# Performance work log

Hardware: AMD Instinct MI355X
Metric: run time of the kernel (lower is better)

## Reference

```python
import jax, jax.numpy as jnp
import numpy as np

N, E, G = 50000, 640000, 2000
F_NODE, F_EDGE, H, L, T = 64, 16, 128, 2, 2


def _seg_softmax(logits, idx, num_seg):
    # logits: [E], idx: [E] -> softmax per segment
    m = jax.ops.segment_max(logits, idx, num_segments=num_seg)
    e = jnp.exp(logits - m[idx])
    s = jax.ops.segment_sum(e, idx, num_segments=num_seg)
    return e / (s[idx] + 1e-16)


def _gru(x, h, Wih, Whh, bih, bhh):
    gi = x @ Wih + bih
    gh = h @ Whh + bhh
    ir, iz, inn = jnp.split(gi, 3, axis=-1)
    hr, hz, hn = jnp.split(gh, 3, axis=-1)
    r = jax.nn.sigmoid(ir + hr)
    z = jax.nn.sigmoid(iz + hz)
    n = jnp.tanh(inn + r * hn)
    return (1.0 - z) * n + z * h


def setup_inputs() -> dict:
    key = jax.random.key(0)
    ks = jax.random.split(key, 30)
    s = 0.05
    inp = {
        'x': jax.random.normal(ks[0], (N, F_NODE), jnp.float32),
        'edge_index': jax.random.randint(ks[1], (2, E), 0, N, jnp.int32),
        'edge_attr': jax.random.normal(ks[2], (E, F_EDGE), jnp.float32),
        'batch': jnp.sort(jax.random.randint(ks[3], (N,), 0, G, jnp.int32)),
        'emb_W': jax.random.normal(ks[4], (F_NODE, H), jnp.float32) * s,
        'emb_b': jnp.zeros((H,), jnp.float32),
        'attW1': jax.random.normal(ks[5], (L, 2 * H + F_EDGE, H), jnp.float32) * s,
        'attb1': jnp.zeros((L, H), jnp.float32),
        'attW2': jax.random.normal(ks[6], (L, H, 1), jnp.float32) * s,
        'attb2': jnp.zeros((L, 1), jnp.float32),
        'mlpW': jax.random.normal(ks[7], (L, H + F_EDGE, H), jnp.float32) * s,
        'mlpb': jnp.zeros((L, H), jnp.float32),
        'gru_Wih': jax.random.normal(ks[8], (L, H, 3 * H), jnp.float32) * s,
        'gru_Whh': jax.random.normal(ks[9], (L, H, 3 * H), jnp.float32) * s,
        'gru_bih': jnp.zeros((L, 3 * H), jnp.float32),
        'gru_bhh': jnp.zeros((L, 3 * H), jnp.float32),
        'gattW1': jax.random.normal(ks[10], (H, H), jnp.float32) * s,
        'gattb1': jnp.zeros((H,), jnp.float32),
        'gattW2': jax.random.normal(ks[11], (H, 1), jnp.float32) * s,
        'gattb2': jnp.zeros((1,), jnp.float32),
        'ggru_Wih': jax.random.normal(ks[12], (H, 3 * H), jnp.float32) * s,
        'ggru_Whh': jax.random.normal(ks[13], (H, 3 * H), jnp.float32) * s,
        'ggru_bih': jnp.zeros((3 * H,), jnp.float32),
        'ggru_bhh': jnp.zeros((3 * H,), jnp.float32),
    }
    return inp


def reference(x, edge_index, edge_attr, batch, emb_W, emb_b, attW1, attb1,
              attW2, attb2, mlpW, mlpb, gru_Wih, gru_Whh, gru_bih, gru_bhh,
              gattW1, gattb1, gattW2, gattb2, ggru_Wih, ggru_Whh, ggru_bih,
              ggru_bhh):
    src, dst = edge_index[0], edge_index[1]  # PyG: x_j = x[src], x_i = x[dst]
    h = jax.nn.relu(x @ emb_W + emb_b)  # [N, H]
    for l in range(L):
        x_i, x_j = h[dst], h[src]                       # [E, H] gathers
        cat = jnp.concatenate([x_i, x_j, edge_attr], axis=-1)  # [E, 2H+F_e]
        a = jax.nn.leaky_relu(cat @ attW1[l] + attb1[l], 0.2) @ attW2[l] + attb2[l]
        alpha = _seg_softmax(a[:, 0], dst, N)[:, None]  # segment softmax over dst
        msg = jax.nn.relu(jnp.concatenate([x_j, edge_attr], axis=-1) @ mlpW[l] + mlpb[l])
        aggr = jax.ops.segment_sum(alpha * msg, dst, num_segments=N)  # [N, H]
        h = _gru(aggr, h, gru_Wih[l], gru_Whh[l], gru_bih[l], gru_bhh[l])
    g = jax.ops.segment_sum(h, batch, num_segments=G)  # global_add_pool [G, H]
    for _ in range(T):
        s = jnp.tanh(h @ gattW1 + gattb1) @ gattW2 + gattb2  # [N, 1]
        att = _seg_softmax(s[:, 0], batch, G)[:, None]
        ctx = jax.ops.segment_sum(att * h, batch, num_segments=G)
        g = _gru(ctx, g, ggru_Wih, ggru_Whh, ggru_bih, ggru_bhh)
    return g
```

## Files before the change

kernel.cpp:

```cpp
#include <hip/hip_runtime.h>
#include <hip/hip_bf16.h>
#include <math.h>

#define N_NODES 50000
#define N_EDGES 640000
#define N_GRAPHS 2000
#define FN 64
#define FE 16
#define H 128
#define NL 2
#define SCB 1024

typedef __attribute__((ext_vector_type(8))) short short8;
typedef __attribute__((ext_vector_type(4))) float float4v;
typedef __hip_bfloat16 bf16;

static constexpr size_t AL = 256;
static constexpr size_t alup(size_t x) { return (x + AL - 1) & ~(AL - 1); }

static constexpr size_t SZ_HF    = (size_t)N_NODES * H * 4;
static constexpr size_t SZ_HB    = (size_t)N_NODES * H * 2;
static constexpr size_t SZ_XB    = (size_t)N_NODES * FN * 2;
static constexpr size_t SZ_PQMB  = (size_t)N_NODES * 384 * 2;
static constexpr size_t SZ_GH    = (size_t)N_NODES * 384 * 4;
static constexpr size_t SZ_GI    = (size_t)N_NODES * 384 * 4;
static constexpr size_t SZ_AGB   = (size_t)N_NODES * H * 2;
static constexpr size_t SZ_NF    = (size_t)N_NODES * 4;
static constexpr size_t SZ_WT    = (size_t)768 * 128 * 2;
static constexpr size_t SZ_WIHT  = (size_t)384 * 128 * 2;
static constexpr size_t SZ_EMBT  = (size_t)128 * 64 * 2;
static constexpr size_t SZ_BBIG  = (size_t)768 * 4;
static constexpr size_t SZ_G128  = (size_t)N_GRAPHS * 128 * 4;
static constexpr size_t SZ_G384  = (size_t)N_GRAPHS * 384 * 4;
static constexpr size_t SZ_GF    = (size_t)N_GRAPHS * 4;
static constexpr size_t SZ_CSE   = (size_t)N_EDGES * 8;
static constexpr size_t SZ_BSUM  = 256 * 4;

static constexpr size_t OFF_H0    = 0;
static constexpr size_t OFF_H1    = alup(OFF_H0 + SZ_HF);
static constexpr size_t OFF_H0B   = alup(OFF_H1 + SZ_HF);
static constexpr size_t OFF_H1B   = alup(OFF_H0B + SZ_HB);
static constexpr size_t OFF_XB    = alup(OFF_H1B + SZ_HB);
static constexpr size_t OFF_PQMB  = alup(OFF_XB + SZ_XB);
static constexpr size_t OFF_GH    = alup(OFF_PQMB + SZ_PQMB);
static constexpr size_t OFF_GI    = alup(OFF_GH + SZ_GH);
static constexpr size_t OFF_AGB   = alup(OFF_GI + SZ_GI);
static constexpr size_t OFF_ES    = alup(OFF_AGB + SZ_AGB);
static constexpr size_t OFF_WT    = alup(OFF_ES + SZ_NF);
static constexpr size_t OFF_WIHT  = alup(OFF_WT + SZ_WT);
static constexpr size_t OFF_EMBT  = alup(OFF_WIHT + SZ_WIHT);
static constexpr size_t OFF_BBIG  = alup(OFF_EMBT + SZ_EMBT);
static constexpr size_t OFF_G0    = alup(OFF_BBIG + SZ_BBIG);
static constexpr size_t OFF_GA    = alup(OFF_G0 + SZ_G128);
static constexpr size_t OFF_CTX   = alup(OFF_GA + SZ_G128);
static constexpr size_t OFF_GICTX = alup(OFF_CTX + SZ_G128);
static constexpr size_t OFF_GHB   = alup(OFF_GICTX + SZ_G384);
static constexpr size_t OFF_GSUM  = alup(OFF_GHB + SZ_G384);
static constexpr size_t OFF_DEG   = alup(OFF_GSUM + SZ_GF);
static constexpr size_t OFF_OFFS  = alup(OFF_DEG + SZ_NF);
static constexpr size_t OFF_CUR   = alup(OFF_OFFS + SZ_NF + 4);
static constexpr size_t OFF_CSE   = alup(OFF_CUR + SZ_NF);
static constexpr size_t OFF_GHIST = alup(OFF_CSE + SZ_CSE);
static constexpr size_t OFF_GOFFS = alup(OFF_GHIST + SZ_GF);
static constexpr size_t OFF_BSUM  = alup(OFF_GOFFS + SZ_GF + 4);
static constexpr size_t TOTAL_WS  = alup(OFF_BSUM + SZ_BSUM);

__device__ unsigned char g_afp_ws[TOTAL_WS];

__device__ inline float bf2f(unsigned short u) {
    unsigned int x = ((unsigned int)u) << 16;
    return __uint_as_float(x);
}

template<int K>
__global__ __launch_bounds__(256) void gemm_mfma(
    const bf16* __restrict__ Abf, const bf16* __restrict__ Btbf,
    const float* __restrict__ bias, float* __restrict__ C,
    bf16* __restrict__ Cb, bf16* __restrict__ Cb2,
    int M, int Ncol, int mode)
{
    const unsigned short* A  = (const unsigned short*)Abf;
    const unsigned short* Bt = (const unsigned short*)Btbf;
    const int l  = threadIdx.x & 63;
    const int w  = threadIdx.x >> 6;
    const int wm = w >> 1, wn = w & 1;
    const int row0 = blockIdx.x * 64 + wm * 32;
    const int col0 = blockIdx.y * 64 + wn * 32;
    const int lr = l & 15;
    const int lk = (l >> 4) * 8;
    float4v acc[2][2] = {};
    #pragma unroll
    for (int k0 = 0; k0 < K; k0 += 32) {
        short8 a[2], b[2];
        #pragma unroll
        for (int i = 0; i < 2; ++i) {
            int r = row0 + i * 16 + lr;
            if (r >= M) r = M - 1;
            a[i] = *(const short8*)(A + (size_t)r * K + k0 + lk);
        }
        #pragma unroll
        for (int j = 0; j < 2; ++j) {
            int c = col0 + j * 16 + lr;
            b[j] = *(const short8*)(Bt + (size_t)c * K + k0 + lk);
        }
        #pragma unroll
        for (int i = 0; i < 2; ++i)
            #pragma unroll
            for (int j = 0; j < 2; ++j)
                acc[i][j] = __builtin_amdgcn_mfma_f32_16x16x32_bf16(a[i], b[j], acc[i][j], 0, 0, 0);
    }
    const int orow = (l >> 4) * 4;
    const int ocol = l & 15;
    #pragma unroll
    for (int i = 0; i < 2; ++i) {
        #pragma unroll
        for (int j = 0; j < 2; ++j) {
            const int gc = col0 + j * 16 + ocol;
            const float bi = bias ? bias[gc] : 0.f;
            #pragma unroll
            for (int r = 0; r < 4; ++r) {
                const int gr = row0 + i * 16 + orow + r;
                if (gr >= M) continue;
                float v = acc[i][j][r] + bi;
                if (mode & 1) v = fmaxf(v, 0.f);
                if (mode & 2) {
                    if (gc < 384) Cb[(size_t)gr * 384 + gc] = __float2bfloat16(v);
                    else          Cb2[(size_t)gr * 384 + (gc - 384)] = __float2bfloat16(v);
                } else if (mode & 8) {
                    Cb[(size_t)gr * Ncol + gc] = __float2bfloat16(v);
                } else {
                    C[(size_t)gr * Ncol + gc] = v;
                    if (mode & 4) Cb[(size_t)gr * Ncol + gc] = __float2bfloat16(v);
                }
            }
        }
    }
}

__global__ __launch_bounds__(256) void gemm_gru(
    const bf16* __restrict__ Abf, const bf16* __restrict__ Btbf,
    const float* __restrict__ bias, const bf16* __restrict__ ghb,
    const bf16* __restrict__ holdb, bf16* __restrict__ hnewb, int M)
{
    const unsigned short* A  = (const unsigned short*)Abf;
    const unsigned short* Bt = (const unsigned short*)Btbf;
    const unsigned short* gh = (const unsigned short*)ghb;
    const unsigned short* hold = (const unsigned short*)holdb;
    const int l  = threadIdx.x & 63;
    const int w  = threadIdx.x >> 6;
    const int row0 = blockIdx.x * 64 + w * 16;
    const int lr = l & 15;
    const int lk = (l >> 4) * 8;
    float4v acc[24] = {};
    #pragma unroll
    for (int k0 = 0; k0 < 128; k0 += 32) {
        int r = row0 + lr;
        if (r >= M) r = M - 1;
        short8 a = *(const short8*)(A + (size_t)r * 128 + k0 + lk);
        #pragma unroll
        for (int j = 0; j < 24; ++j) {
            short8 b = *(const short8*)(Bt + (size_t)(j * 16 + lr) * 128 + k0 + lk);
            acc[j] = __builtin_amdgcn_mfma_f32_16x16x32_bf16(a, b, acc[j], 0, 0, 0);
        }
    }
    const int orow = (l >> 4) * 4;
    const int ocol = l & 15;
    #pragma unroll
    for (int a_ = 0; a_ < 8; ++a_) {
        const int c = a_ * 16 + ocol;
        const float bir = bias[c], biz = bias[c + 128], bin = bias[c + 256];
        #pragma unroll
        for (int r = 0; r < 4; ++r) {
            const int gr = row0 + orow + r;
            if (gr >= M) continue;
            float ir = acc[a_][r] + bir;
            float iz = acc[a_ + 8][r] + biz;
            float in = acc[a_ + 16][r] + bin;
            const unsigned short* ghp = gh + (size_t)gr * 384;
            float hr = bf2f(ghp[c]);
            float hz = bf2f(ghp[128 + c]);
            float hn = bf2f(ghp[256 + c]);
            float rg = 1.f / (1.f + __expf(-(ir + hr)));
            float zg = 1.f / (1.f + __expf(-(iz + hz)));
            float ng = tanhf(in + rg * hn);
            float hv = bf2f(hold[(size_t)gr * 128 + c]);
            float o = (1.f - zg) * ng + zg * hv;
            hnewb[(size_t)gr * 128 + c] = __float2bfloat16(o);
        }
    }
}

#define GBM 64
#define GBN 64
#define GBK 32
__global__ __launch_bounds__(256) void gemm_f32(
    const float* __restrict__ A, const float* __restrict__ B,
    const float* __restrict__ bias, float* __restrict__ C,
    int M, int K, int Ncol)
{
    __shared__ float As[GBK][GBM + 4];
    __shared__ float Bs[GBK][GBN + 4];
    const int tx = threadIdx.x & 15;
    const int ty = threadIdx.x >> 4;
    const int row0 = blockIdx.x * GBM;
    const int col0 = blockIdx.y * GBN;
    float acc[4][4] = {};
    for (int k0 = 0; k0 < K; k0 += GBK) {
        for (int i = threadIdx.x; i < GBM * GBK; i += 256) {
            int r = i / GBK, c = i % GBK;
            float v = 0.f;
            if (row0 + r < M) v = A[(size_t)(row0 + r) * K + k0 + c];
            As[c][r] = v;
        }
        for (int i = threadIdx.x; i < GBK * GBN; i += 256) {
            int r = i / GBN, c = i % GBN;
            float v = 0.f;
            if (col0 + c < Ncol) v = B[(size_t)(k0 + r) * Ncol + col0 + c];
            Bs[r][c] = v;
        }
        __syncthreads();
        #pragma unroll
        for (int k = 0; k < GBK; ++k) {
            float a[4], b[4];
            #pragma unroll
            for (int i = 0; i < 4; ++i) a[i] = As[k][ty * 4 + i];
            #pragma unroll
            for (int j = 0; j < 4; ++j) b[j] = Bs[k][tx * 4 + j];
            #pragma unroll
            for (int i = 0; i < 4; ++i)
                #pragma unroll
                for (int j = 0; j < 4; ++j)
                    acc[i][j] = fmaf(a[i], b[j], acc[i][j]);
        }
        __syncthreads();
    }
    #pragma unroll
    for (int i = 0; i < 4; ++i) {
        int r = row0 + ty * 4 + i;
        if (r >= M) continue;
        #pragma unroll
        for (int j = 0; j < 4; ++j) {
            int c = col0 + tx * 4 + j;
            if (c >= Ncol) continue;
            C[(size_t)r * Ncol + c] = acc[i][j] + (bias ? bias[c] : 0.f);
        }
    }
}

__global__ void pack_weights_bt(const float* __restrict__ attW1,
                                const float* __restrict__ mlpW,
                                const float* __restrict__ whh,
                                const float* __restrict__ attb1,
                                const float* __restrict__ mlpb,
                                const float* __restrict__ bhh,
                                bf16* __restrict__ wt, float* __restrict__ bbig)
{
    int idx = blockIdx.x * blockDim.x + threadIdx.x;
    if (idx >= 768 * 128) return;
    int j = idx >> 7, k = idx & 127;
    float v;
    if (j < 128)      v = attW1[k * 128 + j];
    else if (j < 256) v = attW1[(128 + k) * 128 + (j - 128)];
    else if (j < 384) v = mlpW[k * 128 + (j - 256)];
    else              v = whh[k * 384 + (j - 384)];
    wt[idx] = __float2bfloat16(v);
    if (k == 0) {
        float b;
        if (j < 128)      b = attb1[j];
        else if (j < 256) b = 0.f;
        else if (j < 384) b = mlpb[j - 256];
        else              b = bhh[j - 384];
        bbig[j] = b;
    }
}

__global__ void transpose_cast(const float* __restrict__ in, bf16* __restrict__ out,
                               int K, int Ncol)
{
    int idx = blockIdx.x * blockDim.x + threadIdx.x;
    if (idx >= K * Ncol) return;
    int k = idx / Ncol, j = idx % Ncol;
    out[(size_t)j * K + k] = __float2bfloat16(in[idx]);
}

__global__ void cast_bf16_kernel(const float* __restrict__ in, bf16* __restrict__ out, int n)
{
    int idx = blockIdx.x * blockDim.x + threadIdx.x;
    if (idx < n) out[idx] = __float2bfloat16(in[idx]);
}

__global__ void hist_dst_kernel(const int* __restrict__ ei, int* __restrict__ deg) {
    int e = blockIdx.x * blockDim.x + threadIdx.x;
    if (e < N_EDGES) atomicAdd(&deg[ei[N_EDGES + e]], 1);
}
__global__ void hist_batch_kernel(const int* __restrict__ batch, int* __restrict__ hist) {
    int n = blockIdx.x * blockDim.x + threadIdx.x;
    if (n < N_NODES) atomicAdd(&hist[batch[n]], 1);
}

__global__ __launch_bounds__(1024) void scan_local(const int* __restrict__ in,
        int* __restrict__ out, int* __restrict__ bsum, int n)
{
    __shared__ int buf[SCB];
    int i = blockIdx.x * SCB + threadIdx.x;
    int v = (i < n) ? in[i] : 0;
    buf[threadIdx.x] = v;
    __syncthreads();
    #pragma unroll
    for (int off = 1; off < SCB; off <<= 1) {
        int t = (threadIdx.x >= off) ? buf[threadIdx.x - off] : 0;
        __syncthreads();
        buf[threadIdx.x] += t;
        __syncthreads();
    }
    if (i < n) out[i] = buf[threadIdx.x] - v;
    if (threadIdx.x == SCB - 1) bsum[blockIdx.x] = buf[SCB - 1];
}
__global__ __launch_bounds__(1024) void scan_bsum(int* __restrict__ bsum, int nb,
        int* __restrict__ total_dst)
{
    __shared__ int buf[SCB];
    int v = (threadIdx.x < nb) ? bsum[threadIdx.x] : 0;
    buf[threadIdx.x] = v;
    __syncthreads();
    #pragma unroll
    for (int off = 1; off < SCB; off <<= 1) {
        int t = (threadIdx.x >= off) ? buf[threadIdx.x - off] : 0;
        __syncthreads();
        buf[threadIdx.x] += t;
        __syncthreads();
    }
    if (threadIdx.x < nb) bsum[threadIdx.x] = buf[threadIdx.x] - v;
    if (threadIdx.x == 0) *total_dst = buf[SCB - 1];
}
__global__ __launch_bounds__(1024) void scan_addoff(int* __restrict__ out,
        const int* __restrict__ bsum, int n)
{
    int i = blockIdx.x * SCB + threadIdx.x;
    if (i < n) out[i] += bsum[blockIdx.x];
}

__global__ void scatter_cse_kernel(const int* __restrict__ ei, const int* __restrict__ offs,
                                   int* __restrict__ cur, int2* __restrict__ cse) {
    int e = blockIdx.x * blockDim.x + threadIdx.x;
    if (e >= N_EDGES) return;
    int d = ei[N_EDGES + e];
    int pos = offs[d] + atomicAdd(&cur[d], 1);
    cse[pos] = make_int2(ei[e], e);
}

__global__ __launch_bounds__(256, 2) void edge_fused_kernel(
    const bf16* __restrict__ pqm_b,
    const int2* __restrict__ cse, const float* __restrict__ ea,
    const float* __restrict__ w1c_g, const float* __restrict__ w2_g,
    const float* __restrict__ b2_g, const float* __restrict__ mlpw2_g,
    const int* __restrict__ offs, bf16* __restrict__ aggrb)
{
    const unsigned short* pqm = (const unsigned short*)pqm_b;
    const int wv = threadIdx.x >> 6, lane = threadIdx.x & 63;
    const int c0 = lane * 2;
    float w1r[16][2], wmr[16][2];
    #pragma unroll
    for (int k = 0; k < 16; ++k) {
        w1r[k][0] = w1c_g[k * 128 + c0];
        w1r[k][1] = w1c_g[k * 128 + c0 + 1];
        wmr[k][0] = mlpw2_g[k * 128 + c0];
        wmr[k][1] = mlpw2_g[k * 128 + c0 + 1];
    }
    const float w20 = w2_g[c0], w21 = w2_g[c0 + 1];
    const float b2 = b2_g[0];
    const int d = __builtin_amdgcn_readfirstlane(blockIdx.x * 4 + wv);
    if (d >= N_NODES) return;

    const ushort2 pu = *(const ushort2*)(pqm + (size_t)d * 384 + c0);
    const float p0 = bf2f(pu.x), p1 = bf2f(pu.y);
    float acc0 = 0.f, acc1 = 0.f, ssum = 0.f;
    const int b = offs[d], en = offs[d + 1];
    if (b < en) {
        int2 se = cse[b];
        const unsigned short* ps = pqm + (size_t)se.x * 384;
        ushort2 qu = *(const ushort2*)(ps + 128 + c0);
        ushort2 mu = *(const ushort2*)(ps + 256 + c0);
        const float4* eap = (const float4*)(ea + (size_t)se.y * 16);
        float4 e0 = eap[0], e1 = eap[1], e2 = eap[2], e3 = eap[3];
        for (int i = b; i < en; ++i) {
            float t0 = p0 + bf2f(qu.x), t1 = p1 + bf2f(qu.y);
            float m0 = bf2f(mu.x), m1 = bf2f(mu.y);
            float er[16];
            er[0]=e0.x; er[1]=e0.y; er[2]=e0.z; er[3]=e0.w;
            er[4]=e1.x; er[5]=e1.y; er[6]=e1.z; er[7]=e1.w;
            er[8]=e2.x; er[9]=e2.y; er[10]=e2.z; er[11]=e2.w;
            er[12]=e3.x; er[13]=e3.y; er[14]=e3.z; er[15]=e3.w;
            if (i + 1 < en) {
                se = cse[i + 1];
                const unsigned short* psn = pqm + (size_t)se.x * 384;
                qu = *(const ushort2*)(psn + 128 + c0);
                mu = *(const ushort2*)(psn + 256 + c0);
                const float4* eapn = (const float4*)(ea + (size_t)se.y * 16);
                e0 = eapn[0]; e1 = eapn[1]; e2 = eapn[2]; e3 = eapn[3];
            }
            #pragma unroll
            for (int k = 0; k < 16; ++k) {
                t0 = fmaf(er[k], w1r[k][0], t0);
                t1 = fmaf(er[k], w1r[k][1], t1);
                m0 = fmaf(er[k], wmr[k][0], m0);
                m1 = fmaf(er[k], wmr[k][1], m1);
            }
            float a0 = (t0 > 0.f) ? t0 : 0.2f * t0;
            float a1 = (t1 > 0.f) ? t1 : 0.2f * t1;
            float sp = a0 * w20 + a1 * w21;
            #pragma unroll
            for (int off = 32; off; off >>= 1) sp += __shfl_xor(sp, off);
            const float ex = __expf(sp + b2);
            ssum += ex;
            acc0 = fmaf(ex, fmaxf(m0, 0.f), acc0);
            acc1 = fmaf(ex, fmaxf(m1, 0.f), acc1);
        }
    }
    const float inv = 1.f / (ssum + 1e-16f);
    bf16* outp = aggrb + (size_t)d * 128 + c0;
    outp[0] = __float2bfloat16(acc0 * inv);
    outp[1] = __float2bfloat16(acc1 * inv);
}

__global__ void gru_elem_kernel(const float* __restrict__ gi,
                                const float* __restrict__ gh,
                                const float* __restrict__ hold, float* __restrict__ hnew,
                                int rows)
{
    int idx = blockIdx.x * blockDim.x + threadIdx.x;
    if (idx >= rows * H) return;
    int r = idx >> 7, c = idx & 127;
    float ir = gi[(size_t)r * 384 + c];
    float iz = gi[(size_t)r * 384 + 128 + c];
    float in = gi[(size_t)r * 384 + 256 + c];
    float hr = gh[(size_t)r * 384 + c];
    float hz = gh[(size_t)r * 384 + 128 + c];
    float hn = gh[(size_t)r * 384 + 256 + c];
    float rg = 1.f / (1.f + __expf(-(ir + hr)));
    float zg = 1.f / (1.f + __expf(-(iz + hz)));
    float ng = tanhf(in + rg * hn);
    float hv = hold[idx];
    hnew[idx] = (1.f - zg) * ng + zg * hv;
}

__global__ __launch_bounds__(128) void graph_pool_sum(
    const bf16* __restrict__ hb, const int* __restrict__ goffs, float* __restrict__ g0)
{
    const unsigned short* h = (const unsigned short*)hb;
    int g = blockIdx.x, c = threadIdx.x;
    int b = goffs[g], e2 = goffs[g + 1];
    float acc = 0.f;
    for (int i = b; i < e2; ++i) acc += bf2f(h[(size_t)i * 128 + c]);
    g0[(size_t)g * 128 + c] = acc;
}

__global__ __launch_bounds__(256) void node_score2_kernel(
    const float* __restrict__ hW1, const float* __restrict__ W2,
    const float* __restrict__ b2, const int* __restrict__ batch,
    float* __restrict__ es, float* __restrict__ gsum)
{
    const int wv = threadIdx.x >> 6, lane = threadIdx.x & 63;
    const int n = blockIdx.x * 4 + wv;
    if (n >= N_NODES) return;
    const int c0 = lane * 2;
    float sp = tanhf(hW1[(size_t)n * 128 + c0]) * W2[c0]
             + tanhf(hW1[(size_t)n * 128 + c0 + 1]) * W2[c0 + 1];
    #pragma unroll
    for (int off = 32; off; off >>= 1) sp += __shfl_xor(sp, off);
    if (lane == 0) {
        float ex = __expf(sp + b2[0]);
        es[n] = ex;
        atomicAdd(&gsum[batch[n]], ex);
    }
}

__global__ __launch_bounds__(128) void graph_ctx_kernel(
    const bf16* __restrict__ hb, const int* __restrict__ goffs,
    const float* __restrict__ es, const float* __restrict__ gsum,
    float* __restrict__ ctx)
{
    const unsigned short* h = (const unsigned short*)hb;
    int g = blockIdx.x, c = threadIdx.x;
    float invs = 1.f / (gsum[g] + 1e-16f);
    int b = goffs[g], e2 = goffs[g + 1];
    float acc = 0.f;
    for (int i = b; i < e2; ++i) acc = fmaf(es[i] * invs, bf2f(h[(size_t)i * 128 + c]), acc);
    ctx[(size_t)g * 128 + c] = acc;
}

extern "C" void kernel_launch(void* const* d_in, const int* in_sizes, int n_in,
                              void* d_out, int out_size, void* d_ws, size_t ws_size,
                              hipStream_t stream) {
    const float* x      = (const float*)d_in[0];
    const int*   ei     = (const int*)d_in[1];
    const float* ea     = (const float*)d_in[2];
    const int*   batch  = (const int*)d_in[3];
    const float* embW   = (const float*)d_in[4];
    const float* embB   = (const float*)d_in[5];
    const float* attW1  = (const float*)d_in[6];
    const float* attb1  = (const float*)d_in[7];
    const float* attW2  = (const float*)d_in[8];
    const float* attb2  = (const float*)d_in[9];
    const float* mlpW   = (const float*)d_in[10];
    const float* mlpb   = (const float*)d_in[11];
    const float* gWih   = (const float*)d_in[12];
    const float* gWhh   = (const float*)d_in[13];
    const float* gbih   = (const float*)d_in[14];
    const float* gbhh   = (const float*)d_in[15];
    const float* gattW1 = (const float*)d_in[16];
    const float* gattb1 = (const float*)d_in[17];
    const float* gattW2 = (const float*)d_in[18];
    const float* gattb2 = (const float*)d_in[19];
    const float* ggWih  = (const float*)d_in[20];
    const float* ggWhh  = (const float*)d_in[21];
    const float* ggbih  = (const float*)d_in[22];
    const float* ggbhh  = (const float*)d_in[23];
    float* out = (float*)d_out;

    void* basep = nullptr;
    (void)hipGetSymbolAddress(&basep, HIP_SYMBOL(g_afp_ws));
    char* base = (char*)basep;
    bf16*  h0b   = (bf16*)(base + OFF_H0B);
    bf16*  h1b   = (bf16*)(base + OFF_H1B);
    bf16*  xb    = (bf16*)(base + OFF_XB);
    bf16*  pqmb  = (bf16*)(base + OFF_PQMB);
    bf16*  ghx   = (bf16*)(base + OFF_GH);
    float* hW1   = (float*)(base + OFF_GI);
    bf16*  aggrb = (bf16*)(base + OFF_AGB);
    float* es    = (float*)(base + OFF_ES);
    bf16*  wt    = (bf16*)(base + OFF_WT);
    bf16*  wiht  = (bf16*)(base + OFF_WIHT);
    bf16*  embt  = (bf16*)(base + OFF_EMBT);
    float* bbig  = (float*)(base + OFF_BBIG);
    float* g0b   = (float*)(base + OFF_G0);
    float* gAb   = (float*)(base + OFF_GA);
    float* ctx   = (float*)(base + OFF_CTX);
    float* gictx = (float*)(base + OFF_GICTX);
    float* ghr   = (float*)(base + OFF_GHB);
    float* gsum  = (float*)(base + OFF_GSUM);
    int*   deg   = (int*)(base + OFF_DEG);
    int*   offs  = (int*)(base + OFF_OFFS);
    int*   cur   = (int*)(base + OFF_CUR);
    int2*  cse   = (int2*)(base + OFF_CSE);
    int*   ghist = (int*)(base + OFF_GHIST);
    int*   goffs = (int*)(base + OFF_GOFFS);
    int*   bsum  = (int*)(base + OFF_BSUM);

    (void)hipMemsetAsync(deg, 0, SZ_NF, stream);
    (void)hipMemsetAsync(cur, 0, SZ_NF, stream);
    (void)hipMemsetAsync(ghist, 0, SZ_GF, stream);
    (void)hipMemsetAsync(gsum, 0, SZ_GF, stream);

    const int nbN = (N_NODES + SCB - 1) / SCB;
    const int nbG = (N_GRAPHS + SCB - 1) / SCB;

    hist_dst_kernel<<<(N_EDGES + 255) / 256, 256, 0, stream>>>(ei, deg);
    scan_local<<<nbN, SCB, 0, stream>>>(deg, offs, bsum, N_NODES);
    scan_bsum<<<1, SCB, 0, stream>>>(bsum, nbN, offs + N_NODES);
    scan_addoff<<<nbN, SCB, 0, stream>>>(offs, bsum, N_NODES);
    scatter_cse_kernel<<<(N_EDGES + 255) / 256, 256, 0, stream>>>(ei, offs, cur, cse);
    hist_batch_kernel<<<(N_NODES + 255) / 256, 256, 0, stream>>>(batch, ghist);
    scan_local<<<nbG, SCB, 0, stream>>>(ghist, goffs, bsum, N_GRAPHS);
    scan_bsum<<<1, SCB, 0, stream>>>(bsum, nbG, goffs + N_GRAPHS);
    scan_addoff<<<nbG, SCB, 0, stream>>>(goffs, bsum, N_GRAPHS);

    cast_bf16_kernel<<<(N_NODES * FN + 255) / 256, 256, 0, stream>>>(x, xb, N_NODES * FN);
    transpose_cast<<<(FN * 128 + 255) / 256, 256, 0, stream>>>(embW, embt, FN, 128);

    {
        dim3 g((N_NODES + 63) / 64, 128 / 64);
        gemm_mfma<64><<<g, 256, 0, stream>>>(xb, embt, embB, nullptr, h0b, nullptr,
                                             N_NODES, 128, 1 | 8);
    }

    bf16* hcurb = h0b;
    bf16* hnextb = h1b;
    for (int l = 0; l < NL; ++l) {
        pack_weights_bt<<<(768 * 128 + 255) / 256, 256, 0, stream>>>(
            attW1 + (size_t)l * 272 * 128, mlpW + (size_t)l * 144 * 128,
            gWhh + (size_t)l * 128 * 384, attb1 + l * 128, mlpb + l * 128,
            gbhh + l * 384, wt, bbig);
        {
            dim3 g((N_NODES + 63) / 64, 768 / 64);
            gemm_mfma<128><<<g, 256, 0, stream>>>(hcurb, wt, bbig, nullptr, pqmb, ghx,
                                                  N_NODES, 768, 2);
        }
        edge_fused_kernel<<<(N_NODES + 3) / 4, 256, 0, stream>>>(
            pqmb, cse, ea, attW1 + (size_t)l * 272 * 128 + 256 * 128,
            attW2 + (size_t)l * 128, attb2 + l,
            mlpW + (size_t)l * 144 * 128 + 128 * 128,
            offs, aggrb);
        transpose_cast<<<(128 * 384 + 255) / 256, 256, 0, stream>>>(
            gWih + (size_t)l * 128 * 384, wiht, 128, 384);
        gemm_gru<<<(N_NODES + 63) / 64, 256, 0, stream>>>(
            aggrb, wiht, gbih + l * 384, ghx, hcurb, hnextb, N_NODES);
        bf16* tb = hcurb; hcurb = hnextb; hnextb = tb;
    }

    graph_pool_sum<<<N_GRAPHS, 128, 0, stream>>>(hcurb, goffs, g0b);
    transpose_cast<<<(128 * 128 + 255) / 256, 256, 0, stream>>>(gattW1, wiht, 128, 128);
    {
        dim3 g((N_NODES + 63) / 64, 128 / 64);
        gemm_mfma<128><<<g, 256, 0, stream>>>(hcurb, wiht, gattb1, hW1, nullptr, nullptr,
                                              N_NODES, 128, 0);
    }
    node_score2_kernel<<<(N_NODES + 3) / 4, 256, 0, stream>>>(
        hW1, gattW2, gattb2, batch, es, gsum);
    graph_ctx_kernel<<<N_GRAPHS, 128, 0, stream>>>(hcurb, goffs, es, gsum, ctx);

    dim3 gg((N_GRAPHS + 63) / 64, 384 / 64);
    gemm_f32<<<gg, 256, 0, stream>>>(ctx, ggWih, ggbih, gictx, N_GRAPHS, H, 384);
    gemm_f32<<<gg, 256, 0, stream>>>(g0b, ggWhh, ggbhh, ghr, N_GRAPHS, H, 384);
    gru_elem_kernel<<<((size_t)N_GRAPHS * H + 255) / 256, 256, 0, stream>>>(
        gictx, ghr, g0b, gAb, N_GRAPHS);
    gemm_f32<<<gg, 256, 0, stream>>>(gAb, ggWhh, ggbhh, ghr, N_GRAPHS, H, 384);
    gru_elem_kernel<<<((size_t)N_GRAPHS * H + 255) / 256, 256, 0, stream>>>(
        gictx, ghr, gAb, out, N_GRAPHS);
}
```

Before: 916.3 us.

## Reorder edge attrs into CSR order, interleave q/m columns, pack edge weights

The scatter step now writes edge attributes into a dst-sorted contiguous buffer, so the edge kernel reads them sequentially instead of gathering by edge id. The GEMM output interleaves the q and m columns so one 8-byte load fetches both per lane. The edge weights are pre-packed as float4 per lane, and the edge loop processes four edges per batch so four shuffle reductions run together. The attention score GEMM output becomes bf16 and the memsets are merged into one, trading an extra copy of the edge attributes and lower-precision hW1 for less scattered memory traffic.

```diff
diff --git a/kernel.cpp b/kernel.cpp
--- a/kernel.cpp
+++ b/kernel.cpp
@@ -18,51 +18,53 @@
 static constexpr size_t AL = 256;
 static constexpr size_t alup(size_t x) { return (x + AL - 1) & ~(AL - 1); }
 
-static constexpr size_t SZ_HF    = (size_t)N_NODES * H * 4;
 static constexpr size_t SZ_HB    = (size_t)N_NODES * H * 2;
 static constexpr size_t SZ_XB    = (size_t)N_NODES * FN * 2;
 static constexpr size_t SZ_PQMB  = (size_t)N_NODES * 384 * 2;
-static constexpr size_t SZ_GH    = (size_t)N_NODES * 384 * 4;
-static constexpr size_t SZ_GI    = (size_t)N_NODES * 384 * 4;
+static constexpr size_t SZ_GHX   = (size_t)N_NODES * 384 * 2;
+static constexpr size_t SZ_HW1B  = (size_t)N_NODES * H * 2;
 static constexpr size_t SZ_AGB   = (size_t)N_NODES * H * 2;
 static constexpr size_t SZ_NF    = (size_t)N_NODES * 4;
 static constexpr size_t SZ_WT    = (size_t)768 * 128 * 2;
 static constexpr size_t SZ_WIHT  = (size_t)384 * 128 * 2;
 static constexpr size_t SZ_EMBT  = (size_t)128 * 64 * 2;
+static constexpr size_t SZ_WPK   = (size_t)16 * 256 * 4;
 static constexpr size_t SZ_BBIG  = (size_t)768 * 4;
 static constexpr size_t SZ_G128  = (size_t)N_GRAPHS * 128 * 4;
 static constexpr size_t SZ_G384  = (size_t)N_GRAPHS * 384 * 4;
 static constexpr size_t SZ_GF    = (size_t)N_GRAPHS * 4;
-static constexpr size_t SZ_CSE   = (size_t)N_EDGES * 8;
+static constexpr size_t SZ_CSRC  = (size_t)N_EDGES * 4 + 64;
+static constexpr size_t SZ_EAC   = (size_t)N_EDGES * 64;
 static constexpr size_t SZ_BSUM  = 256 * 4;
 
-static constexpr size_t OFF_H0    = 0;
-static constexpr size_t OFF_H1    = alup(OFF_H0 + SZ_HF);
-static constexpr size_t OFF_H0B   = alup(OFF_H1 + SZ_HF);
+static constexpr size_t OFF_H0B   = 0;
 static constexpr size_t OFF_H1B   = alup(OFF_H0B + SZ_HB);
 static constexpr size_t OFF_XB    = alup(OFF_H1B + SZ_HB);
 static constexpr size_t OFF_PQMB  = alup(OFF_XB + SZ_XB);
-static constexpr size_t OFF_GH    = alup(OFF_PQMB + SZ_PQMB);
-static constexpr size_t OFF_GI    = alup(OFF_GH + SZ_GH);
-static constexpr size_t OFF_AGB   = alup(OFF_GI + SZ_GI);
+static constexpr size_t OFF_GHX   = alup(OFF_PQMB + SZ_PQMB);
+static constexpr size_t OFF_HW1B  = alup(OFF_GHX + SZ_GHX);
+static constexpr size_t OFF_AGB   = alup(OFF_HW1B + SZ_HW1B);
 static constexpr size_t OFF_ES    = alup(OFF_AGB + SZ_AGB);
 static constexpr size_t OFF_WT    = alup(OFF_ES + SZ_NF);
 static constexpr size_t OFF_WIHT  = alup(OFF_WT + SZ_WT);
 static constexpr size_t OFF_EMBT  = alup(OFF_WIHT + SZ_WIHT);
-static constexpr size_t OFF_BBIG  = alup(OFF_EMBT + SZ_EMBT);
+static constexpr size_t OFF_WPK   = alup(OFF_EMBT + SZ_EMBT);
+static constexpr size_t OFF_BBIG  = alup(OFF_WPK + SZ_WPK);
 static constexpr size_t OFF_G0    = alup(OFF_BBIG + SZ_BBIG);
 static constexpr size_t OFF_GA    = alup(OFF_G0 + SZ_G128);
 static constexpr size_t OFF_CTX   = alup(OFF_GA + SZ_G128);
 static constexpr size_t OFF_GICTX = alup(OFF_CTX + SZ_G128);
-static constexpr size_t OFF_GHB   = alup(OFF_GICTX + SZ_G384);
-static constexpr size_t OFF_GSUM  = alup(OFF_GHB + SZ_G384);
-static constexpr size_t OFF_DEG   = alup(OFF_GSUM + SZ_GF);
-static constexpr size_t OFF_OFFS  = alup(OFF_DEG + SZ_NF);
-static constexpr size_t OFF_CUR   = alup(OFF_OFFS + SZ_NF + 4);
-static constexpr size_t OFF_CSE   = alup(OFF_CUR + SZ_NF);
-static constexpr size_t OFF_GHIST = alup(OFF_CSE + SZ_CSE);
-static constexpr size_t OFF_GOFFS = alup(OFF_GHIST + SZ_GF);
-static constexpr size_t OFF_BSUM  = alup(OFF_GOFFS + SZ_GF + 4);
+static constexpr size_t OFF_GHR   = alup(OFF_GICTX + SZ_G384);
+static constexpr size_t OFF_DEG   = alup(OFF_GHR + SZ_G384);
+static constexpr size_t OFF_CUR   = alup(OFF_DEG + SZ_NF);
+static constexpr size_t OFF_GHIST = alup(OFF_CUR + SZ_NF);
+static constexpr size_t OFF_GSUM  = alup(OFF_GHIST + SZ_GF);
+static constexpr size_t SZ_ZERO   = OFF_GSUM + SZ_GF - OFF_DEG;
+static constexpr size_t OFF_OFFS  = alup(OFF_GSUM + SZ_GF);
+static constexpr size_t OFF_GOFFS = alup(OFF_OFFS + SZ_NF + 4);
+static constexpr size_t OFF_CSRC  = alup(OFF_GOFFS + SZ_GF + 4);
+static constexpr size_t OFF_EAC   = alup(OFF_CSRC + SZ_CSRC);
+static constexpr size_t OFF_BSUM  = alup(OFF_EAC + SZ_EAC);
 static constexpr size_t TOTAL_WS  = alup(OFF_BSUM + SZ_BSUM);
 
 __device__ unsigned char g_afp_ws[TOTAL_WS];
@@ -124,13 +126,21 @@
                 float v = acc[i][j][r] + bi;
                 if (mode & 1) v = fmaxf(v, 0.f);
                 if (mode & 2) {
-                    if (gc < 384) Cb[(size_t)gr * 384 + gc] = __float2bfloat16(v);
-                    else          Cb2[(size_t)gr * 384 + (gc - 384)] = __float2bfloat16(v);
+                    if (gc < 128) {
+                        Cb[(size_t)gr * 384 + gc] = __float2bfloat16(v);
+                    } else if (gc < 256) {
+                        int c = gc - 128;
+                        Cb[(size_t)gr * 384 + 128 + ((c >> 1) << 2) + (c & 1)] = __float2bfloat16(v);
+                    } else if (gc < 384) {
+                        int c = gc - 256;
+                        Cb[(size_t)gr * 384 + 128 + ((c >> 1) << 2) + 2 + (c & 1)] = __float2bfloat16(v);
+                    } else {
+                        Cb2[(size_t)gr * 384 + (gc - 384)] = __float2bfloat16(v);
+                    }
                 } else if (mode & 8) {
                     Cb[(size_t)gr * Ncol + gc] = __float2bfloat16(v);
                 } else {
                     C[(size_t)gr * Ncol + gc] = v;
-                    if (mode & 4) Cb[(size_t)gr * Ncol + gc] = __float2bfloat16(v);
                 }
             }
         }
@@ -274,6 +284,17 @@
     }
 }
 
+__global__ void pack_edge_w(const float* __restrict__ w1c, const float* __restrict__ wm,
+                            float* __restrict__ wpack)
+{
+    int idx = blockIdx.x * blockDim.x + threadIdx.x;
+    if (idx >= 16 * 256) return;
+    int k = idx >> 8, j = idx & 255;
+    int l = j >> 2, q = j & 3;
+    float v = (q < 2) ? w1c[k * 128 + 2 * l + q] : wm[k * 128 + 2 * l + (q - 2)];
+    wpack[idx] = v;
+}
+
 __global__ void transpose_cast(const float* __restrict__ in, bf16* __restrict__ out,
                                int K, int Ncol)
 {
@@ -340,36 +361,39 @@
     if (i < n) out[i] += bsum[blockIdx.x];
 }
 
-__global__ void scatter_cse_kernel(const int* __restrict__ ei, const int* __restrict__ offs,
-                                   int* __restrict__ cur, int2* __restrict__ cse) {
+__global__ void scatter_cse_kernel(const int* __restrict__ ei, const float* __restrict__ ea,
+                                   const int* __restrict__ offs, int* __restrict__ cur,
+                                   int* __restrict__ csrc, float* __restrict__ eac) {
     int e = blockIdx.x * blockDim.x + threadIdx.x;
     if (e >= N_EDGES) return;
     int d = ei[N_EDGES + e];
     int pos = offs[d] + atomicAdd(&cur[d], 1);
-    cse[pos] = make_int2(ei[e], e);
-}
-
-__global__ __launch_bounds__(256, 2) void edge_fused_kernel(
+    csrc[pos] = ei[e];
+    const float4* src = (const float4*)(ea + (size_t)e * 16);
+    float4* dst = (float4*)(eac + (size_t)pos * 16);
+    dst[0] = src[0]; dst[1] = src[1]; dst[2] = src[2]; dst[3] = src[3];
+}
+
+__global__ __launch_bounds__(256) void edge_fused_kernel(
     const bf16* __restrict__ pqm_b,
-    const int2* __restrict__ cse, const float* __restrict__ ea,
-    const float* __restrict__ w1c_g, const float* __restrict__ w2_g,
-    const float* __restrict__ b2_g, const float* __restrict__ mlpw2_g,
+    const int* __restrict__ csrc, const float* __restrict__ eac,
+    const float* __restrict__ wpack, const float* __restrict__ w2_g,
+    const float* __restrict__ b2_g,
     const int* __restrict__ offs, bf16* __restrict__ aggrb)
 {
     const unsigned short* pqm = (const unsigned short*)pqm_b;
     const int wv = threadIdx.x >> 6, lane = threadIdx.x & 63;
     const int c0 = lane * 2;
-    float w1r[16][2], wmr[16][2];
-    #pragma unroll
-    for (int k = 0; k < 16; ++k) {
-        w1r[k][0] = w1c_g[k * 128 + c0];
-        w1r[k][1] = w1c_g[k * 128 + c0 + 1];
-        wmr[k][0] = mlpw2_g[k * 128 + c0];
-        wmr[k][1] = mlpw2_g[k * 128 + c0 + 1];
-    }
+    float4 wreg[16];
+    #pragma unroll
+    for (int k = 0; k < 16; ++k)
+        wreg[k] = *(const float4*)(wpack + k * 256 + lane * 4);
+    #pragma unroll
+    for (int k = 0; k < 16; ++k)
+        asm volatile("" : "+v"(wreg[k].x), "+v"(wreg[k].y), "+v"(wreg[k].z), "+v"(wreg[k].w));
     const float w20 = w2_g[c0], w21 = w2_g[c0 + 1];
     const float b2 = b2_g[0];
-    const int d = __builtin_amdgcn_readfirstlane(blockIdx.x * 4 + wv);
+    const int d = blockIdx.x * 4 + wv;
     if (d >= N_NODES) return;
 
     const ushort2 pu = *(const ushort2*)(pqm + (size_t)d * 384 + c0);
@@ -377,44 +401,59 @@
     float acc0 = 0.f, acc1 = 0.f, ssum = 0.f;
     const int b = offs[d], en = offs[d + 1];
     if (b < en) {
-        int2 se = cse[b];
-        const unsigned short* ps = pqm + (size_t)se.x * 384;
-        ushort2 qu = *(const ushort2*)(ps + 128 + c0);
-        ushort2 mu = *(const ushort2*)(ps + 256 + c0);
-        const float4* eap = (const float4*)(ea + (size_t)se.y * 16);
-        float4 e0 = eap[0], e1 = eap[1], e2 = eap[2], e3 = eap[3];
-        for (int i = b; i < en; ++i) {
-            float t0 = p0 + bf2f(qu.x), t1 = p1 + bf2f(qu.y);
-            float m0 = bf2f(mu.x), m1 = bf2f(mu.y);
-            float er[16];
-            er[0]=e0.x; er[1]=e0.y; er[2]=e0.z; er[3]=e0.w;
-            er[4]=e1.x; er[5]=e1.y; er[6]=e1.z; er[7]=e1.w;
-            er[8]=e2.x; er[9]=e2.y; er[10]=e2.z; er[11]=e2.w;
-            er[12]=e3.x; er[13]=e3.y; er[14]=e3.z; er[15]=e3.w;
-            if (i + 1 < en) {
-                se = cse[i + 1];
-                const unsigned short* psn = pqm + (size_t)se.x * 384;
-                qu = *(const ushort2*)(psn + 128 + c0);
-                mu = *(const ushort2*)(psn + 256 + c0);
-                const float4* eapn = (const float4*)(ea + (size_t)se.y * 16);
-                e0 = eapn[0]; e1 = eapn[1]; e2 = eapn[2]; e3 = eapn[3];
+        int s = csrc[b];
+        ushort4 qm = *(const ushort4*)(pqm + (size_t)s * 384 + 128 + lane * 4);
+        const float4* ep = (const float4*)(eac + (size_t)b * 16);
+        float4 e0 = ep[0], e1 = ep[1], e2 = ep[2], e3 = ep[3];
+        int i = b;
+        while (i < en) {
+            float sp4[4], m04[4], m14[4];
+            #pragma unroll
+            for (int t = 0; t < 4; ++t) {
+                if (i + t < en) {
+                    float t0 = p0 + bf2f(qm.x), t1 = p1 + bf2f(qm.y);
+                    float m0 = bf2f(qm.z), m1 = bf2f(qm.w);
+                    float er[16];
+                    er[0]=e0.x; er[1]=e0.y; er[2]=e0.z; er[3]=e0.w;
+                    er[4]=e1.x; er[5]=e1.y; er[6]=e1.z; er[7]=e1.w;
+                    er[8]=e2.x; er[9]=e2.y; er[10]=e2.z; er[11]=e2.w;
+                    er[12]=e3.x; er[13]=e3.y; er[14]=e3.z; er[15]=e3.w;
+                    if (i + t + 1 < en) {
+                        s = csrc[i + t + 1];
+                        qm = *(const ushort4*)(pqm + (size_t)s * 384 + 128 + lane * 4);
+                        const float4* epn = (const float4*)(eac + (size_t)(i + t + 1) * 16);
+                        e0 = epn[0]; e1 = epn[1]; e2 = epn[2]; e3 = epn[3];
+                    }
+                    #pragma unroll
+                    for (int k = 0; k < 16; ++k) {
+                        t0 = fmaf(er[k], wreg[k].x, t0);
+                        t1 = fmaf(er[k], wreg[k].y, t1);
+                        m0 = fmaf(er[k], wreg[k].z, m0);
+                        m1 = fmaf(er[k], wreg[k].w, m1);
+                    }
+                    float a0 = (t0 > 0.f) ? t0 : 0.2f * t0;
+                    float a1 = (t1 > 0.f) ? t1 : 0.2f * t1;
+                    sp4[t] = a0 * w20 + a1 * w21;
+                    m04[t] = m0; m14[t] = m1;
+                } else {
+                    sp4[t] = -1e30f; m04[t] = 0.f; m14[t] = 0.f;
+                }
             }
             #pragma unroll
-            for (int k = 0; k < 16; ++k) {
-                t0 = fmaf(er[k], w1r[k][0], t0);
-                t1 = fmaf(er[k], w1r[k][1], t1);
-                m0 = fmaf(er[k], wmr[k][0], m0);
-                m1 = fmaf(er[k], wmr[k][1], m1);
+            for (int off = 32; off; off >>= 1) {
+                sp4[0] += __shfl_xor(sp4[0], off);
+                sp4[1] += __shfl_xor(sp4[1], off);
+                sp4[2] += __shfl_xor(sp4[2], off);
+                sp4[3] += __shfl_xor(sp4[3], off);
             }
-            float a0 = (t0 > 0.f) ? t0 : 0.2f * t0;
-            float a1 = (t1 > 0.f) ? t1 : 0.2f * t1;
-            float sp = a0 * w20 + a1 * w21;
-            #pragma unroll
-            for (int off = 32; off; off >>= 1) sp += __shfl_xor(sp, off);
-            const float ex = __expf(sp + b2);
-            ssum += ex;
-            acc0 = fmaf(ex, fmaxf(m0, 0.f), acc0);
-            acc1 = fmaf(ex, fmaxf(m1, 0.f), acc1);
+            #pragma unroll
+            for (int t = 0; t < 4; ++t) {
+                const float ex = __expf(sp4[t] + b2);
+                ssum += ex;
+                acc0 = fmaf(ex, fmaxf(m04[t], 0.f), acc0);
+                acc1 = fmaf(ex, fmaxf(m14[t], 0.f), acc1);
+            }
+            i += 4;
         }
     }
     const float inv = 1.f / (ssum + 1e-16f);
@@ -456,16 +495,17 @@
 }
 
 __global__ __launch_bounds__(256) void node_score2_kernel(
-    const float* __restrict__ hW1, const float* __restrict__ W2,
+    const bf16* __restrict__ hW1b, const float* __restrict__ W2,
     const float* __restrict__ b2, const int* __restrict__ batch,
     float* __restrict__ es, float* __restrict__ gsum)
 {
+    const unsigned short* hW1 = (const unsigned short*)hW1b;
     const int wv = threadIdx.x >> 6, lane = threadIdx.x & 63;
     const int n = blockIdx.x * 4 + wv;
     if (n >= N_NODES) return;
     const int c0 = lane * 2;
-    float sp = tanhf(hW1[(size_t)n * 128 + c0]) * W2[c0]
-             + tanhf(hW1[(size_t)n * 128 + c0 + 1]) * W2[c0 + 1];
+    ushort2 hv = *(const ushort2*)(hW1 + (size_t)n * 128 + c0);
+    float sp = tanhf(bf2f(hv.x)) * W2[c0] + tanhf(bf2f(hv.y)) * W2[c0 + 1];
     #pragma unroll
     for (int off = 32; off; off >>= 1) sp += __shfl_xor(sp, off);
     if (lane == 0) {
@@ -525,32 +565,31 @@
     bf16*  h1b   = (bf16*)(base + OFF_H1B);
     bf16*  xb    = (bf16*)(base + OFF_XB);
     bf16*  pqmb  = (bf16*)(base + OFF_PQMB);
-    bf16*  ghx   = (bf16*)(base + OFF_GH);
-    float* hW1   = (float*)(base + OFF_GI);
+    bf16*  ghx   = (bf16*)(base + OFF_GHX);
+    bf16*  hW1b  = (bf16*)(base + OFF_HW1B);
     bf16*  aggrb = (bf16*)(base + OFF_AGB);
     float* es    = (float*)(base + OFF_ES);
     bf16*  wt    = (bf16*)(base + OFF_WT);
     bf16*  wiht  = (bf16*)(base + OFF_WIHT);
     bf16*  embt  = (bf16*)(base + OFF_EMBT);
+    float* wpack = (float*)(base + OFF_WPK);
     float* bbig  = (float*)(base + OFF_BBIG);
     float* g0b   = (float*)(base + OFF_G0);
     float* gAb   = (float*)(base + OFF_GA);
     float* ctx   = (float*)(base + OFF_CTX);
     float* gictx = (float*)(base + OFF_GICTX);
-    float* ghr   = (float*)(base + OFF_GHB);
+    float* ghr   = (float*)(base + OFF_GHR);
+    int*   deg   = (int*)(base + OFF_DEG);
+    int*   cur   = (int*)(base + OFF_CUR);
+    int*   ghist = (int*)(base + OFF_GHIST);
     float* gsum  = (float*)(base + OFF_GSUM);
-    int*   deg   = (int*)(base + OFF_DEG);
     int*   offs  = (int*)(base + OFF_OFFS);
-    int*   cur   = (int*)(base + OFF_CUR);
-    int2*  cse   = (int2*)(base + OFF_CSE);
-    int*   ghist = (int*)(base + OFF_GHIST);
     int*   goffs = (int*)(base + OFF_GOFFS);
+    int*   csrc  = (int*)(base + OFF_CSRC);
+    float* eac   = (float*)(base + OFF_EAC);
     int*   bsum  = (int*)(base + OFF_BSUM);
 
-    (void)hipMemsetAsync(deg, 0, SZ_NF, stream);
-    (void)hipMemsetAsync(cur, 0, SZ_NF, stream);
-    (void)hipMemsetAsync(ghist, 0, SZ_GF, stream);
-    (void)hipMemsetAsync(gsum, 0, SZ_GF, stream);
+    (void)hipMemsetAsync(deg, 0, SZ_ZERO, stream);
 
     const int nbN = (N_NODES + SCB - 1) / SCB;
     const int nbG = (N_GRAPHS + SCB - 1) / SCB;
@@ -559,7 +598,7 @@
     scan_local<<<nbN, SCB, 0, stream>>>(deg, offs, bsum, N_NODES);
     scan_bsum<<<1, SCB, 0, stream>>>(bsum, nbN, offs + N_NODES);
     scan_addoff<<<nbN, SCB, 0, stream>>>(offs, bsum, N_NODES);
-    scatter_cse_kernel<<<(N_EDGES + 255) / 256, 256, 0, stream>>>(ei, offs, cur, cse);
+    scatter_cse_kernel<<<(N_EDGES + 255) / 256, 256, 0, stream>>>(ei, ea, offs, cur, csrc, eac);
     hist_batch_kernel<<<(N_NODES + 255) / 256, 256, 0, stream>>>(batch, ghist);
     scan_local<<<nbG, SCB, 0, stream>>>(ghist, goffs, bsum, N_GRAPHS);
     scan_bsum<<<1, SCB, 0, stream>>>(bsum, nbG, goffs + N_GRAPHS);
@@ -581,15 +620,16 @@
             attW1 + (size_t)l * 272 * 128, mlpW + (size_t)l * 144 * 128,
             gWhh + (size_t)l * 128 * 384, attb1 + l * 128, mlpb + l * 128,
             gbhh + l * 384, wt, bbig);
+        pack_edge_w<<<16, 256, 0, stream>>>(
+            attW1 + (size_t)l * 272 * 128 + 256 * 128,
+            mlpW + (size_t)l * 144 * 128 + 128 * 128, wpack);
         {
             dim3 g((N_NODES + 63) / 64, 768 / 64);
             gemm_mfma<128><<<g, 256, 0, stream>>>(hcurb, wt, bbig, nullptr, pqmb, ghx,
                                                   N_NODES, 768, 2);
         }
         edge_fused_kernel<<<(N_NODES + 3) / 4, 256, 0, stream>>>(
-            pqmb, cse, ea, attW1 + (size_t)l * 272 * 128 + 256 * 128,
-            attW2 + (size_t)l * 128, attb2 + l,
-            mlpW + (size_t)l * 144 * 128 + 128 * 128,
+            pqmb, csrc, eac, wpack, attW2 + (size_t)l * 128, attb2 + l,
             offs, aggrb);
         transpose_cast<<<(128 * 384 + 255) / 256, 256, 0, stream>>>(
             gWih + (size_t)l * 128 * 384, wiht, 128, 384);
@@ -602,11 +642,11 @@
     transpose_cast<<<(128 * 128 + 255) / 256, 256, 0, stream>>>(gattW1, wiht, 128, 128);
     {
         dim3 g((N_NODES + 63) / 64, 128 / 64);
-        gemm_mfma<128><<<g, 256, 0, stream>>>(hcurb, wiht, gattb1, hW1, nullptr, nullptr,
-                                              N_NODES, 128, 0);
+        gemm_mfma<128><<<g, 256, 0, stream>>>(hcurb, wiht, gattb1, nullptr, hW1b, nullptr,
+                                              N_NODES, 128, 8);
     }
     node_score2_kernel<<<(N_NODES + 3) / 4, 256, 0, stream>>>(
-        hW1, gattW2, gattb2, batch, es, gsum);
+        hW1b, gattW2, gattb2, batch, es, gsum);
     graph_ctx_kernel<<<N_GRAPHS, 128, 0, stream>>>(hcurb, goffs, es, gsum, ctx);
 
     dim3 gg((N_GRAPHS + 63) / 64, 384 / 64);
```

After: 1.270 ms. 38.6% more time.
